# Kernel optimization log

Hardware: AMD Instinct MI355X
Metric: run time of the kernel (lower is better)

The kernel has to match this reference:

```python
import jax, jax.numpy as jnp
import numpy as np

T_STEPS, N, STATE, HID, ACT, C = 32, 64, 64, 128, 32, 96


def setup_inputs() -> dict:
    key = jax.random.key(0)
    ks = jax.random.split(key, 16)
    s = 0.05
    inp = {
        'x': jax.random.normal(ks[0], (T_STEPS, N, STATE), jnp.float32),
        'a': jax.random.normal(ks[1], (T_STEPS, N, ACT), jnp.float32),
        # GRU layer 0 (input state_dim) and layer 1 (input hidden_dim)
        'wih0': jax.random.normal(ks[2], (3 * HID, STATE), jnp.float32) * s,
        'whh0': jax.random.normal(ks[3], (3 * HID, HID), jnp.float32) * s,
        'bih0': jax.random.normal(ks[4], (3 * HID,), jnp.float32) * s,
        'bhh0': jax.random.normal(ks[5], (3 * HID,), jnp.float32) * s,
        'wih1': jax.random.normal(ks[6], (3 * HID, HID), jnp.float32) * s,
        'whh1': jax.random.normal(ks[7], (3 * HID, HID), jnp.float32) * s,
        'bih1': jax.random.normal(ks[8], (3 * HID,), jnp.float32) * s,
        'bhh1': jax.random.normal(ks[9], (3 * HID,), jnp.float32) * s,
        'w1': jax.random.normal(ks[10], (HID, HID + ACT), jnp.float32) * s,
        'b1': jax.random.normal(ks[11], (HID,), jnp.float32) * s,
        'w2': jax.random.normal(ks[12], (1, 2 * HID), jnp.float32) * s,
        'b2': jax.random.normal(ks[13], (1,), jnp.float32) * s,
        'Tm': jax.random.normal(ks[14], (HID, HID, C), jnp.float32),  # init.normal(T,0,1)
    }
    return inp


def _gru_cell(x_t, h, wih, whh, bih, bhh):
    gi = x_t @ wih.T + bih            # (N, 3H)
    gh = h @ whh.T + bhh
    i_r, i_z, i_n = jnp.split(gi, 3, axis=-1)
    h_r, h_z, h_n = jnp.split(gh, 3, axis=-1)
    r = jax.nn.sigmoid(i_r + h_r)
    z = jax.nn.sigmoid(i_z + h_z)
    n = jnp.tanh(i_n + r * h_n)
    return (1.0 - z) * n + z * h


def reference(x, a, wih0, whh0, bih0, bhh0, wih1, whh1, bih1, bhh1, w1, b1, w2, b2, Tm):
    def step(h, x_t):
        h0 = _gru_cell(x_t, h[0], wih0, whh0, bih0, bhh0)
        h1 = _gru_cell(h0, h[1], wih1, whh1, bih1, bhh1)
        return jnp.stack([h0, h1]), h1

    h_init = jnp.zeros((2, N, HID), x.dtype)
    _, p = jax.lax.scan(step, h_init, x)              # (T, N, H)

    fc1 = jax.nn.relu(jnp.concatenate([p, a], -1) @ w1.T + b1)  # (T, N, H)

    Tflat = Tm.reshape(HID, HID * C)

    def batch_discrim(xt):  # xt: (N, H)
        M = (xt @ Tflat).reshape(N, HID, C)           # (N, B, C)
        # pairwise L1 over C: (N, N, B)
        norm = jnp.abs(M[:, None] - M[None, :]).sum(-1)
        o_b = (jnp.exp(-norm).sum(0) - 1.0) / (N - 1)  # (N, B)
        return jnp.concatenate([xt, o_b], 1)          # (N, 2H)

    fc2 = jax.lax.map(batch_discrim, fc1)             # (T, N, 2H)
    prob = jax.nn.sigmoid(fc2 @ w2.T + b2)            # (T, N, 1)
    return prob
```

## Files before the change

kernel.cpp:

```cpp
#include <hip/hip_runtime.h>
#include <hip/hip_fp16.h>
#include <cstdint>

#define T_STEPS 32
#define NB 64
#define STATE 64
#define HID 128
#define ACT 32
#define CDIM 96
#define G3 (3*HID)

typedef __attribute__((ext_vector_type(8))) short short8;
typedef __attribute__((ext_vector_type(4))) float f32x4;
typedef _Float16 h2v __attribute__((ext_vector_type(2)));

__device__ __forceinline__ unsigned short f2bf(float f){
  unsigned int u = __builtin_bit_cast(unsigned int, f);
  u = u + 0x7FFFu + ((u >> 16) & 1u);
  return (unsigned short)(u >> 16);
}
__device__ __forceinline__ unsigned int packh2(float f0, float f1){
  return (unsigned int)__half_as_ushort(__float2half_rn(f0)) |
         ((unsigned int)__half_as_ushort(__float2half_rn(f1)) << 16);
}
__device__ __forceinline__ float sigmoidf_(float x){ return 1.0f/(1.0f + __expf(-x)); }
__device__ __forceinline__ float tanhf_(float x){ float e = __expf(2.0f*x); return (e-1.0f)/(e+1.0f); }

__device__ __forceinline__ float dot2f(float acc, unsigned int a, unsigned int b){
  h2v av = __builtin_bit_cast(h2v, a);
  h2v bv = __builtin_bit_cast(h2v, b);
  return __builtin_amdgcn_fdot2(av, bv, acc, false);
}
__device__ __forceinline__ float l1d(float acc, unsigned int ua, unsigned int ub){
  __half2 a = __builtin_bit_cast(__half2, ua);
  __half2 b = __builtin_bit_cast(__half2, ub);
  __half2 d = __habs2(__hsub2(a, b));
  h2v dv = __builtin_bit_cast(h2v, d);
  h2v ones; ones[0] = (_Float16)1.0f; ones[1] = (_Float16)1.0f;
  return __builtin_amdgcn_fdot2(dv, ones, acc, false);
}
__device__ __forceinline__ float l1d4(float acc, uint4 a, uint4 b){
  acc = l1d(acc, a.x, b.x); acc = l1d(acc, a.y, b.y);
  acc = l1d(acc, a.z, b.z); acc = l1d(acc, a.w, b.w);
  return acc;
}

__global__ void k_prep(const float* __restrict__ Tm, unsigned short* __restrict__ tmh,
                       const float* __restrict__ wih0, const float* __restrict__ whh0,
                       const float* __restrict__ wih1, const float* __restrict__ whh1,
                       const float* __restrict__ w1,
                       unsigned int* __restrict__ wih0p, unsigned int* __restrict__ whh0p,
                       unsigned int* __restrict__ wih1p, unsigned int* __restrict__ whh1p,
                       unsigned int* __restrict__ w1p){
  int tid = threadIdx.x;
  if (blockIdx.x < 128){
    int b = blockIdx.x;
    for (int e = tid; e < HID*CDIM; e += 256){
      int chunk = e / 768;
      int r1 = e - chunk*768;
      int c = r1 >> 3, h = r1 & 7;
      int k = chunk*8 + h;
      tmh[b*(HID*CDIM) + e] = f2bf(Tm[k*(HID*CDIM) + b*CDIM + c]);
    }
  } else {
    int mb = blockIdx.x - 128;
    const float* srcs[5] = {wih0, whh0, wih1, whh1, w1};
    unsigned int* dsts[5] = {wih0p, whh0p, wih1p, whh1p, w1p};
    const int Rs[5]  = {384,384,384,384,128};
    const int K2s[5] = {32,64,64,64,80};
    for (int mm = 0; mm < 5; mm++){
      const float* s = srcs[mm]; unsigned int* d = dsts[mm];
      int R = Rs[mm], K2 = K2s[mm], tot = R*K2;
      for (int e = mb*256 + tid; e < tot; e += 8*256){
        int k2 = e / R, r = e - k2*R;
        d[e] = packh2(s[r*(2*K2) + 2*k2], s[r*(2*K2) + 2*k2 + 1]);
      }
    }
  }
}

__global__ __launch_bounds__(768) void k_gru0(const float* __restrict__ x,
                                              const unsigned int* __restrict__ wih0p,
                                              const unsigned int* __restrict__ whh0p,
                                              const unsigned int* __restrict__ wih1p,
                                              const float* __restrict__ bih0, const float* __restrict__ bhh0,
                                              const float* __restrict__ bih1,
                                              float* __restrict__ gi1g){
  __shared__ __align__(16) unsigned int hl2[64];
  __shared__ __align__(16) unsigned int xall[1024];
  __shared__ float ghl[G3], gil[G3];
  int n = blockIdx.x, tid = threadIdx.x;
  int r = tid >> 1, kh = tid & 1;
  unsigned int wi0[16], wh0[32], wi1[32];
  #pragma unroll
  for (int i = 0; i < 16; i++) wi0[i] = wih0p[(kh*16 + i)*384 + r];
  #pragma unroll
  for (int i = 0; i < 32; i++) wh0[i] = whh0p[(kh*32 + i)*384 + r];
  #pragma unroll
  for (int i = 0; i < 32; i++) wi1[i] = wih1p[(kh*32 + i)*384 + r];
  float bh0 = (kh == 0) ? bhh0[r] : 0.0f;
  float bi0 = (kh == 0) ? bih0[r] : 0.0f;
  float bi1 = (kh == 0) ? bih1[r] : 0.0f;
  for (int e = tid; e < 1024; e += 768){
    int t_ = e >> 5, i = e & 31;
    const float* xp = x + t_*(NB*STATE) + n*STATE + 2*i;
    xall[e] = packh2(xp[0], xp[1]);
  }
  if (tid < 64) hl2[tid] = 0u;
  float hprev = 0.0f;
  __syncthreads();
  const uint4* hl4 = (const uint4*)hl2;
  for (int t = 0; t <= T_STEPS; t++){
    float gh = bh0, gi1 = bi1, gi0 = bi0;
    #pragma unroll
    for (int g = 0; g < 2; g++){
      uint4 hv[4];
      #pragma unroll
      for (int j = 0; j < 4; j++) hv[j] = hl4[kh*8 + g*4 + j];
      #pragma unroll
      for (int j = 0; j < 4; j++){
        gh = dot2f(gh, wh0[g*16 + j*4 + 0], hv[j].x);
        gh = dot2f(gh, wh0[g*16 + j*4 + 1], hv[j].y);
        gh = dot2f(gh, wh0[g*16 + j*4 + 2], hv[j].z);
        gh = dot2f(gh, wh0[g*16 + j*4 + 3], hv[j].w);
        gi1 = dot2f(gi1, wi1[g*16 + j*4 + 0], hv[j].x);
        gi1 = dot2f(gi1, wi1[g*16 + j*4 + 1], hv[j].y);
        gi1 = dot2f(gi1, wi1[g*16 + j*4 + 2], hv[j].z);
        gi1 = dot2f(gi1, wi1[g*16 + j*4 + 3], hv[j].w);
      }
    }
    if (t < T_STEPS){
      const uint4* xl4 = (const uint4*)&xall[t*32];
      #pragma unroll
      for (int j = 0; j < 4; j++){
        uint4 xv = xl4[kh*4 + j];
        gi0 = dot2f(gi0, wi0[j*4 + 0], xv.x);
        gi0 = dot2f(gi0, wi0[j*4 + 1], xv.y);
        gi0 = dot2f(gi0, wi0[j*4 + 2], xv.z);
        gi0 = dot2f(gi0, wi0[j*4 + 3], xv.w);
      }
    }
    gh  += __shfl_xor(gh, 1);
    gi1 += __shfl_xor(gi1, 1);
    gi0 += __shfl_xor(gi0, 1);
    if (kh == 0){
      if (t < T_STEPS){ ghl[r] = gh; gil[r] = gi0; }
      if (t >= 1) gi1g[((t-1)*NB + n)*G3 + r] = gi1;
    }
    __syncthreads();
    if (t < T_STEPS && tid < HID){
      float rg = sigmoidf_(gil[tid]       + ghl[tid]);
      float z  = sigmoidf_(gil[tid+HID]   + ghl[tid+HID]);
      float nn = tanhf_   (gil[tid+2*HID] + rg*ghl[tid+2*HID]);
      float hn = (1.0f - z)*nn + z*hprev;
      hprev = hn;
      ((__half*)hl2)[tid] = __float2half_rn(hn);
    }
    __syncthreads();
  }
}

__global__ __launch_bounds__(768) void k_gru1(const float* __restrict__ a,
                                              const unsigned int* __restrict__ whh1p,
                                              const unsigned int* __restrict__ w1p,
                                              const float* __restrict__ bhh1, const float* __restrict__ b1,
                                              const float* __restrict__ gi1g,
                                              float* __restrict__ fc1f, unsigned short* __restrict__ fc1h){
  __shared__ __align__(16) unsigned int hl2[64];
  __shared__ __align__(16) unsigned int aall[512];
  __shared__ float ghl[G3];
  int n = blockIdx.x, tid = threadIdx.x;
  int r = tid >> 1, kh = tid & 1;
  unsigned int wh1[32];
  #pragma unroll
  for (int i = 0; i < 32; i++) wh1[i] = whh1p[(kh*32 + i)*384 + r];
  unsigned int w1h[32], w1a[8];
  if (r < HID){
    #pragma unroll
    for (int i = 0; i < 32; i++) w1h[i] = w1p[(kh*32 + i)*128 + r];
    #pragma unroll
    for (int i = 0; i < 8; i++)  w1a[i] = w1p[(64 + kh*8 + i)*128 + r];
  }
  float bh1 = (kh == 0) ? bhh1[r] : 0.0f;
  float bf1 = (kh == 0 && r < HID) ? b1[r] : 0.0f;
  for (int e = tid; e < 512; e += 768){
    int t_ = e >> 4, i = e & 15;
    const float* ap = a + t_*(NB*ACT) + n*ACT + 2*i;
    aall[e] = packh2(ap[0], ap[1]);
  }
  if (tid < 64) hl2[tid] = 0u;
  float hprev = 0.0f;
  float g_r = 0.0f, g_z = 0.0f, g_n = 0.0f;
  if (tid < HID){
    const float* gp = gi1g + n*G3 + tid;
    g_r = gp[0]; g_z = gp[HID]; g_n = gp[2*HID];
  }
  __syncthreads();
  const uint4* hl4 = (const uint4*)hl2;
  for (int t = 0; t <= T_STEPS; t++){
    float gh = bh1, fc = bf1;
    bool dofc = (r < HID) && (t >= 1);
    #pragma unroll
    for (int g = 0; g < 2; g++){
      uint4 hv[4];
      #pragma unroll
      for (int j = 0; j < 4; j++) hv[j] = hl4[kh*8 + g*4 + j];
      #pragma unroll
      for (int j = 0; j < 4; j++){
        gh = dot2f(gh, wh1[g*16 + j*4 + 0], hv[j].x);
        gh = dot2f(gh, wh1[g*16 + j*4 + 1], hv[j].y);
        gh = dot2f(gh, wh1[g*16 + j*4 + 2], hv[j].z);
        gh = dot2f(gh, wh1[g*16 + j*4 + 3], hv[j].w);
      }
      if (dofc){
        #pragma unroll
        for (int j = 0; j < 4; j++){
          fc = dot2f(fc, w1h[g*16 + j*4 + 0], hv[j].x);
          fc = dot2f(fc, w1h[g*16 + j*4 + 1], hv[j].y);
          fc = dot2f(fc, w1h[g*16 + j*4 + 2], hv[j].z);
          fc = dot2f(fc, w1h[g*16 + j*4 + 3], hv[j].w);
        }
      }
    }
    if (dofc){
      const uint4* al4 = (const uint4*)&aall[(t-1)*16];
      #pragma unroll
      for (int j = 0; j < 2; j++){
        uint4 av = al4[kh*2 + j];
        fc = dot2f(fc, w1a[j*4 + 0], av.x);
        fc = dot2f(fc, w1a[j*4 + 1], av.y);
        fc = dot2f(fc, w1a[j*4 + 2], av.z);
        fc = dot2f(fc, w1a[j*4 + 3], av.w);
      }
    }
    gh += __shfl_xor(gh, 1);
    fc += __shfl_xor(fc, 1);
    if (kh == 0){
      if (t < T_STEPS) ghl[r] = gh;
      if (t >= 1 && r < HID){
        float v = fmaxf(fc, 0.0f);
        fc1f[((t-1)*NB + n)*HID + r] = v;
        fc1h[(t-1)*8192 + (n>>4)*2048 + (r>>3)*128 + (n&15)*8 + (r&7)] = f2bf(v);
      }
    }
    __syncthreads();
    if (t < T_STEPS && tid < HID){
      float cr = g_r, cz = g_z, cn = g_n;
      int tn2 = (t+1 < T_STEPS) ? t+1 : t;
      const float* gp = gi1g + (tn2*NB + n)*G3 + tid;
      g_r = gp[0]; g_z = gp[HID]; g_n = gp[2*HID];
      float rg = sigmoidf_(cr + ghl[tid]);
      float z  = sigmoidf_(cz + ghl[tid+HID]);
      float nn = tanhf_   (cn + rg*ghl[tid+2*HID]);
      float hn = (1.0f - z)*nn + z*hprev;
      hprev = hn;
      ((__half*)hl2)[tid] = __float2half_rn(hn);
    }
    __syncthreads();
  }
}

__global__ __launch_bounds__(256) void k_disc(const unsigned short* __restrict__ fc1h,
                                              const unsigned short* __restrict__ tmh,
                                              float* __restrict__ O){
  __shared__ __align__(16) __half Mh[64*104];
  __shared__ float ps[64*18];
  int b = blockIdx.x, t = blockIdx.y;
  int tid = threadIdx.x;
  int wave = tid >> 6, lane = tid & 63, m = lane & 15, quad = lane >> 4;
  const uint4* Ag = (const uint4*)(fc1h + t*8192);
  const uint4* Bg = (const uint4*)(tmh + b*(CDIM*HID));
  uint4 a4[4];
  #pragma unroll
  for (int kk = 0; kk < 4; kk++) a4[kk] = Ag[wave*256 + (kk*4 + quad)*16 + m];
  f32x4 acc[6];
  #pragma unroll
  for (int i = 0; i < 6; i++) acc[i] = (f32x4)(0.0f);
  #pragma unroll
  for (int kk = 0; kk < 4; kk++){
    short8 av = __builtin_bit_cast(short8, a4[kk]);
    #pragma unroll
    for (int nt = 0; nt < 6; nt++){
      uint4 b4 = Bg[(kk*4 + quad)*96 + nt*16 + m];
      acc[nt] = __builtin_amdgcn_mfma_f32_16x16x32_bf16(av, __builtin_bit_cast(short8, b4), acc[nt], 0, 0, 0);
    }
  }
  #pragma unroll
  for (int nt = 0; nt < 6; nt++){
    #pragma unroll
    for (int rr = 0; rr < 4; rr++){
      Mh[(rr*16 + wave*4 + quad)*104 + nt*16 + m] = __float2half(acc[nt][rr]);
    }
  }
  __syncthreads();
  const uint4* M4 = (const uint4*)Mh;
  if (tid < 240){
    int chalf = tid & 1, tp = tid >> 1;
    int rnd = tp >> 3, slot = tp & 7;
    int ta, tb;
    if (slot == 0){ ta = 15; tb = rnd; }
    else {
      ta = rnd + slot;      if (ta >= 15) ta -= 15;
      tb = rnd + 15 - slot; if (tb >= 15) tb -= 15;
    }
    float facc[16];
    #pragma unroll
    for (int p = 0; p < 16; p++) facc[p] = 0.0f;
    auto doChunk = [&](int c){
      int ch = chalf*6 + c;
      uint4 av[4], bv[4];
      #pragma unroll
      for (int s = 0; s < 4; s++){
        av[s] = M4[(s*16 + ta)*13 + ch];
        bv[s] = M4[(s*16 + tb)*13 + ch];
      }
      #pragma unroll
      for (int i = 0; i < 4; i++)
        #pragma unroll
        for (int j = 0; j < 4; j++)
          facc[i*4+j] = l1d4(facc[i*4+j], av[i], bv[j]);
    };
    doChunk(0); doChunk(1);
    bool big1 = true;
    #pragma unroll
    for (int p = 0; p < 16; p++) big1 = big1 && (facc[p] > 14.0f);
    if (!big1){
      doChunk(2); doChunk(3);
      bool big2 = true;
      #pragma unroll
      for (int p = 0; p < 16; p++) big2 = big2 && (facc[p] > 14.0f);
      if (!big2){ doChunk(4); doChunk(5); }
    }
    float tot[16];
    #pragma unroll
    for (int p = 0; p < 16; p++) tot[p] = facc[p] + __shfl_xor(facc[p], 1);
    if (chalf == 0){
      #pragma unroll
      for (int i = 0; i < 4; i++){
        float s = 0.0f;
        #pragma unroll
        for (int j = 0; j < 4; j++) s += __expf(-tot[i*4+j]);
        ps[(ta*4 + i)*18 + tb] = s;
      }
    } else {
      #pragma unroll
      for (int j = 0; j < 4; j++){
        float s = 0.0f;
        #pragma unroll
        for (int i = 0; i < 4; i++) s += __expf(-tot[i*4+j]);
        ps[(tb*4 + j)*18 + ta] = s;
      }
    }
  } else {
    int ta = tid - 240;
    float f6[6];
    #pragma unroll
    for (int p = 0; p < 6; p++) f6[p] = 0.0f;
    auto doChunkS = [&](int ch){
      uint4 rv[4];
      #pragma unroll
      for (int s = 0; s < 4; s++) rv[s] = M4[(s*16 + ta)*13 + ch];
      f6[0] = l1d4(f6[0], rv[0], rv[1]);
      f6[1] = l1d4(f6[1], rv[0], rv[2]);
      f6[2] = l1d4(f6[2], rv[0], rv[3]);
      f6[3] = l1d4(f6[3], rv[1], rv[2]);
      f6[4] = l1d4(f6[4], rv[1], rv[3]);
      f6[5] = l1d4(f6[5], rv[2], rv[3]);
    };
    doChunkS(0); doChunkS(1); doChunkS(2);
    bool big1 = true;
    #pragma unroll
    for (int p = 0; p < 6; p++) big1 = big1 && (f6[p] > 14.0f);
    if (!big1){
      doChunkS(3); doChunkS(4); doChunkS(5);
      bool big2 = true;
      #pragma unroll
      for (int p = 0; p < 6; p++) big2 = big2 && (f6[p] > 14.0f);
      if (!big2){
        doChunkS(6); doChunkS(7); doChunkS(8);
        doChunkS(9); doChunkS(10); doChunkS(11);
      }
    }
    float e01 = __expf(-f6[0]), e02 = __expf(-f6[1]), e03 = __expf(-f6[2]);
    float e12 = __expf(-f6[3]), e13 = __expf(-f6[4]), e23 = __expf(-f6[5]);
    ps[(ta*4 + 0)*18 + ta] = e01 + e02 + e03;
    ps[(ta*4 + 1)*18 + ta] = e01 + e12 + e13;
    ps[(ta*4 + 2)*18 + ta] = e02 + e12 + e23;
    ps[(ta*4 + 3)*18 + ta] = e03 + e13 + e23;
  }
  __syncthreads();
  if (tid < NB){
    float s = 0.0f;
    #pragma unroll
    for (int k = 0; k < 16; k++) s += ps[tid*18 + k];
    O[(t*HID + b)*NB + tid] = s*(1.0f/63.0f);
  }
}

__global__ __launch_bounds__(256) void k_final(const float* __restrict__ fc1f, const float* __restrict__ O,
                                               const float* __restrict__ w2, const float* __restrict__ b2,
                                               float* __restrict__ out){
  __shared__ float ol[NB*HID];
  __shared__ float fl[NB*130];
  __shared__ float wl[2*HID + 2];
  int t = blockIdx.x, tid = threadIdx.x;
  for (int i = tid; i < NB*HID; i += 256) ol[i] = O[t*NB*HID + i];
  for (int i = tid; i < NB*HID; i += 256){ int n = i >> 7, h = i & 127; fl[n*130 + h] = fc1f[t*NB*HID + i]; }
  if (tid < 2*HID) wl[tid] = w2[tid];
  if (tid == 0) wl[2*HID] = b2[0];
  __syncthreads();
  if (tid < NB){
    float acc = wl[2*HID];
    #pragma unroll 8
    for (int h = 0; h < HID; h++) acc += fl[tid*130 + h]*wl[h];
    #pragma unroll 8
    for (int b = 0; b < HID; b++) acc += ol[b*NB + tid]*wl[HID + b];
    out[t*NB + tid] = sigmoidf_(acc);
  }
}

extern "C" void kernel_launch(void* const* d_in, const int* in_sizes, int n_in,
                              void* d_out, int out_size, void* d_ws, size_t ws_size,
                              hipStream_t stream){
  const float* x    = (const float*)d_in[0];
  const float* a    = (const float*)d_in[1];
  const float* wih0 = (const float*)d_in[2];
  const float* whh0 = (const float*)d_in[3];
  const float* bih0 = (const float*)d_in[4];
  const float* bhh0 = (const float*)d_in[5];
  const float* wih1 = (const float*)d_in[6];
  const float* whh1 = (const float*)d_in[7];
  const float* bih1 = (const float*)d_in[8];
  const float* bhh1 = (const float*)d_in[9];
  const float* w1   = (const float*)d_in[10];
  const float* b1   = (const float*)d_in[11];
  const float* w2   = (const float*)d_in[12];
  const float* b2   = (const float*)d_in[13];
  const float* Tm   = (const float*)d_in[14];
  float* ws = (float*)d_ws;
  float* gi1g = ws;
  float* fc1f = ws + 786432;
  float* Ows  = ws + 1048576;
  unsigned short* fc1h = (unsigned short*)(ws + 1310720);
  unsigned short* tmh  = (unsigned short*)(ws + 1441792);
  unsigned int* wih0p = (unsigned int*)(ws + 2228224);
  unsigned int* whh0p = (unsigned int*)(ws + 2240512);
  unsigned int* wih1p = (unsigned int*)(ws + 2265088);
  unsigned int* whh1p = (unsigned int*)(ws + 2289664);
  unsigned int* w1p   = (unsigned int*)(ws + 2314240);
  float* out = (float*)d_out;

  k_prep<<<dim3(136), dim3(256), 0, stream>>>(Tm, tmh, wih0, whh0, wih1, whh1, w1,
                                              wih0p, whh0p, wih1p, whh1p, w1p);
  k_gru0<<<dim3(NB), dim3(768), 0, stream>>>(x, wih0p, whh0p, wih1p, bih0, bhh0, bih1, gi1g);
  k_gru1<<<dim3(NB), dim3(768), 0, stream>>>(a, whh1p, w1p, bhh1, b1, gi1g, fc1f, fc1h);
  k_disc<<<dim3(HID, T_STEPS), dim3(256), 0, stream>>>(fc1h, tmh, Ows);
  k_final<<<dim3(T_STEPS), dim3(256), 0, stream>>>(fc1f, Ows, w2, b2, out);
}
```

Measured before the change: 212.8 us.

## Fuse both GRU layers into one kernel and move fc1 to an MFMA kernel

Merges the two GRU recurrence kernels into a single per-sample kernel that runs both layers each timestep. This removes the gi1 global round trip and one launch, but adds an extra barrier phase per step and more register pressure from holding four weight sets. The fc1 layer now runs as a separate bf16 MFMA kernel over all timesteps, with the action inputs prepacked in k_prep. k_disc processes 4 timesteps per block, which reuses the Tm tile but gives fewer blocks, and k_final reads the bf16 fc1 output instead of a float copy.

```diff
diff --git a/kernel.cpp b/kernel.cpp
--- a/kernel.cpp
+++ b/kernel.cpp
@@ -19,6 +19,9 @@
   u = u + 0x7FFFu + ((u >> 16) & 1u);
   return (unsigned short)(u >> 16);
 }
+__device__ __forceinline__ float bf2f(unsigned short u){
+  unsigned int v = ((unsigned int)u) << 16; return __builtin_bit_cast(float, v);
+}
 __device__ __forceinline__ unsigned int packh2(float f0, float f1){
   return (unsigned int)__half_as_ushort(__float2half_rn(f0)) |
          ((unsigned int)__half_as_ushort(__float2half_rn(f1)) << 16);
@@ -48,13 +51,14 @@
 __global__ void k_prep(const float* __restrict__ Tm, unsigned short* __restrict__ tmh,
                        const float* __restrict__ wih0, const float* __restrict__ whh0,
                        const float* __restrict__ wih1, const float* __restrict__ whh1,
-                       const float* __restrict__ w1,
+                       const float* __restrict__ w1, const float* __restrict__ a,
                        unsigned int* __restrict__ wih0p, unsigned int* __restrict__ whh0p,
                        unsigned int* __restrict__ wih1p, unsigned int* __restrict__ whh1p,
-                       unsigned int* __restrict__ w1p){
+                       unsigned short* __restrict__ w1f, unsigned short* __restrict__ h1af){
   int tid = threadIdx.x;
-  if (blockIdx.x < 128){
-    int b = blockIdx.x;
+  int bx = blockIdx.x;
+  if (bx < 128){
+    int b = bx;
     for (int e = tid; e < HID*CDIM; e += 256){
       int chunk = e / 768;
       int r1 = e - chunk*768;
@@ -62,201 +66,178 @@
       int k = chunk*8 + h;
       tmh[b*(HID*CDIM) + e] = f2bf(Tm[k*(HID*CDIM) + b*CDIM + c]);
     }
+  } else if (bx < 136){
+    int mb = bx - 128;
+    const float* srcs[4] = {wih0, whh0, wih1, whh1};
+    unsigned int* dsts[4] = {wih0p, whh0p, wih1p, whh1p};
+    const int K2s[4] = {32,64,64,64};
+    for (int mm = 0; mm < 4; mm++){
+      const float* s = srcs[mm]; unsigned int* d = dsts[mm];
+      int K2 = K2s[mm], tot = 384*K2;
+      for (int e = mb*256 + tid; e < tot; e += 8*256){
+        int k2 = e / 384, r = e - k2*384;
+        d[e] = packh2(s[r*(2*K2) + 2*k2], s[r*(2*K2) + 2*k2 + 1]);
+      }
+    }
+  } else if (bx < 140){
+    int mb = bx - 136;
+    for (int e = mb*256 + tid; e < 20480; e += 4*256){
+      int kchunk = e >> 10, rem = e & 1023;
+      int col = rem >> 3, j = rem & 7;
+      w1f[e] = f2bf(w1[col*160 + kchunk*8 + j]);
+    }
   } else {
-    int mb = blockIdx.x - 128;
-    const float* srcs[5] = {wih0, whh0, wih1, whh1, w1};
-    unsigned int* dsts[5] = {wih0p, whh0p, wih1p, whh1p, w1p};
-    const int Rs[5]  = {384,384,384,384,128};
-    const int K2s[5] = {32,64,64,64,80};
-    for (int mm = 0; mm < 5; mm++){
-      const float* s = srcs[mm]; unsigned int* d = dsts[mm];
-      int R = Rs[mm], K2 = K2s[mm], tot = R*K2;
-      for (int e = mb*256 + tid; e < tot; e += 8*256){
-        int k2 = e / R, r = e - k2*R;
-        d[e] = packh2(s[r*(2*K2) + 2*k2], s[r*(2*K2) + 2*k2 + 1]);
-      }
-    }
-  }
-}
-
-__global__ __launch_bounds__(768) void k_gru0(const float* __restrict__ x,
-                                              const unsigned int* __restrict__ wih0p,
-                                              const unsigned int* __restrict__ whh0p,
-                                              const unsigned int* __restrict__ wih1p,
-                                              const float* __restrict__ bih0, const float* __restrict__ bhh0,
-                                              const float* __restrict__ bih1,
-                                              float* __restrict__ gi1g){
-  __shared__ __align__(16) unsigned int hl2[64];
+    int mb = bx - 140;
+    for (int e = mb*256 + tid; e < 65536; e += 12*256){
+      int t = e >> 11, rem = e & 2047;
+      int n = rem >> 5, c = rem & 31;
+      int pos = t*10240 + (n>>4)*2560 + (16 + (c>>3))*128 + (n&15)*8 + (c&7);
+      h1af[pos] = f2bf(a[t*(NB*ACT) + n*ACT + c]);
+    }
+  }
+}
+
+__global__ __launch_bounds__(768, 3) void k_gruF(const float* __restrict__ x,
+                                                 const unsigned int* __restrict__ wih0p,
+                                                 const unsigned int* __restrict__ whh0p,
+                                                 const unsigned int* __restrict__ wih1p,
+                                                 const unsigned int* __restrict__ whh1p,
+                                                 const float* __restrict__ bih0, const float* __restrict__ bhh0,
+                                                 const float* __restrict__ bih1, const float* __restrict__ bhh1,
+                                                 unsigned short* __restrict__ h1af){
+  __shared__ __align__(16) unsigned int h0l[64];
+  __shared__ __align__(16) unsigned int h1l[64];
   __shared__ __align__(16) unsigned int xall[1024];
-  __shared__ float ghl[G3], gil[G3];
+  __shared__ float A0[G3], B0[G3], C1[G3];
   int n = blockIdx.x, tid = threadIdx.x;
   int r = tid >> 1, kh = tid & 1;
-  unsigned int wi0[16], wh0[32], wi1[32];
+  unsigned int wi0[16], wh0[32], wi1[32], wh1[32];
   #pragma unroll
   for (int i = 0; i < 16; i++) wi0[i] = wih0p[(kh*16 + i)*384 + r];
   #pragma unroll
   for (int i = 0; i < 32; i++) wh0[i] = whh0p[(kh*32 + i)*384 + r];
   #pragma unroll
   for (int i = 0; i < 32; i++) wi1[i] = wih1p[(kh*32 + i)*384 + r];
-  float bh0 = (kh == 0) ? bhh0[r] : 0.0f;
-  float bi0 = (kh == 0) ? bih0[r] : 0.0f;
-  float bi1 = (kh == 0) ? bih1[r] : 0.0f;
+  #pragma unroll
+  for (int i = 0; i < 32; i++) wh1[i] = whh1p[(kh*32 + i)*384 + r];
+  float bh0v = (kh == 0) ? bhh0[r] : 0.0f;
+  float bi0v = (kh == 0) ? bih0[r] : 0.0f;
+  float bi1v = (kh == 0) ? bih1[r] : 0.0f;
+  float bh1v = (kh == 0) ? bhh1[r] : 0.0f;
   for (int e = tid; e < 1024; e += 768){
     int t_ = e >> 5, i = e & 31;
     const float* xp = x + t_*(NB*STATE) + n*STATE + 2*i;
     xall[e] = packh2(xp[0], xp[1]);
   }
-  if (tid < 64) hl2[tid] = 0u;
-  float hprev = 0.0f;
+  if (tid < 64){ h0l[tid] = 0u; h1l[tid] = 0u; }
+  float h0prev = 0.0f, h1prev = 0.0f;
   __syncthreads();
-  const uint4* hl4 = (const uint4*)hl2;
-  for (int t = 0; t <= T_STEPS; t++){
-    float gh = bh0, gi1 = bi1, gi0 = bi0;
+  const uint4* h04 = (const uint4*)h0l;
+  const uint4* h14 = (const uint4*)h1l;
+  const uint4* xl4 = (const uint4*)xall;
+  for (int t = 0; t < T_STEPS; t++){
+    float gh0 = bh0v, gi0 = bi0v, gh1 = bh1v;
+    #pragma unroll
+    for (int g = 0; g < 2; g++){
+      uint4 hv0[4], hv1[4];
+      #pragma unroll
+      for (int j = 0; j < 4; j++){ hv0[j] = h04[kh*8 + g*4 + j]; hv1[j] = h14[kh*8 + g*4 + j]; }
+      #pragma unroll
+      for (int j = 0; j < 4; j++){
+        gh0 = dot2f(gh0, wh0[g*16 + j*4 + 0], hv0[j].x);
+        gh0 = dot2f(gh0, wh0[g*16 + j*4 + 1], hv0[j].y);
+        gh0 = dot2f(gh0, wh0[g*16 + j*4 + 2], hv0[j].z);
+        gh0 = dot2f(gh0, wh0[g*16 + j*4 + 3], hv0[j].w);
+        gh1 = dot2f(gh1, wh1[g*16 + j*4 + 0], hv1[j].x);
+        gh1 = dot2f(gh1, wh1[g*16 + j*4 + 1], hv1[j].y);
+        gh1 = dot2f(gh1, wh1[g*16 + j*4 + 2], hv1[j].z);
+        gh1 = dot2f(gh1, wh1[g*16 + j*4 + 3], hv1[j].w);
+      }
+    }
+    #pragma unroll
+    for (int j = 0; j < 4; j++){
+      uint4 xv = xl4[t*8 + kh*4 + j];
+      gi0 = dot2f(gi0, wi0[j*4 + 0], xv.x);
+      gi0 = dot2f(gi0, wi0[j*4 + 1], xv.y);
+      gi0 = dot2f(gi0, wi0[j*4 + 2], xv.z);
+      gi0 = dot2f(gi0, wi0[j*4 + 3], xv.w);
+    }
+    gh0 += __shfl_xor(gh0, 1);
+    gi0 += __shfl_xor(gi0, 1);
+    gh1 += __shfl_xor(gh1, 1);
+    if (kh == 0){ A0[r] = gh0; B0[r] = gi0; C1[r] = gh1; }
+    __syncthreads();
+    if (tid < HID){
+      float rg = sigmoidf_(B0[tid]       + A0[tid]);
+      float z  = sigmoidf_(B0[tid+HID]   + A0[tid+HID]);
+      float nn = tanhf_   (B0[tid+2*HID] + rg*A0[tid+2*HID]);
+      float hn = (1.0f - z)*nn + z*h0prev;
+      h0prev = hn;
+      ((__half*)h0l)[tid] = __float2half_rn(hn);
+    }
+    __syncthreads();
+    float gi1 = bi1v;
     #pragma unroll
     for (int g = 0; g < 2; g++){
       uint4 hv[4];
       #pragma unroll
-      for (int j = 0; j < 4; j++) hv[j] = hl4[kh*8 + g*4 + j];
+      for (int j = 0; j < 4; j++) hv[j] = h04[kh*8 + g*4 + j];
       #pragma unroll
       for (int j = 0; j < 4; j++){
-        gh = dot2f(gh, wh0[g*16 + j*4 + 0], hv[j].x);
-        gh = dot2f(gh, wh0[g*16 + j*4 + 1], hv[j].y);
-        gh = dot2f(gh, wh0[g*16 + j*4 + 2], hv[j].z);
-        gh = dot2f(gh, wh0[g*16 + j*4 + 3], hv[j].w);
         gi1 = dot2f(gi1, wi1[g*16 + j*4 + 0], hv[j].x);
         gi1 = dot2f(gi1, wi1[g*16 + j*4 + 1], hv[j].y);
         gi1 = dot2f(gi1, wi1[g*16 + j*4 + 2], hv[j].z);
         gi1 = dot2f(gi1, wi1[g*16 + j*4 + 3], hv[j].w);
       }
     }
-    if (t < T_STEPS){
-      const uint4* xl4 = (const uint4*)&xall[t*32];
-      #pragma unroll
-      for (int j = 0; j < 4; j++){
-        uint4 xv = xl4[kh*4 + j];
-        gi0 = dot2f(gi0, wi0[j*4 + 0], xv.x);
-        gi0 = dot2f(gi0, wi0[j*4 + 1], xv.y);
-        gi0 = dot2f(gi0, wi0[j*4 + 2], xv.z);
-        gi0 = dot2f(gi0, wi0[j*4 + 3], xv.w);
-      }
-    }
-    gh  += __shfl_xor(gh, 1);
     gi1 += __shfl_xor(gi1, 1);
-    gi0 += __shfl_xor(gi0, 1);
-    if (kh == 0){
-      if (t < T_STEPS){ ghl[r] = gh; gil[r] = gi0; }
-      if (t >= 1) gi1g[((t-1)*NB + n)*G3 + r] = gi1;
-    }
-    __syncthreads();
-    if (t < T_STEPS && tid < HID){
-      float rg = sigmoidf_(gil[tid]       + ghl[tid]);
-      float z  = sigmoidf_(gil[tid+HID]   + ghl[tid+HID]);
-      float nn = tanhf_   (gil[tid+2*HID] + rg*ghl[tid+2*HID]);
-      float hn = (1.0f - z)*nn + z*hprev;
-      hprev = hn;
-      ((__half*)hl2)[tid] = __float2half_rn(hn);
-    }
-    __syncthreads();
-  }
-}
-
-__global__ __launch_bounds__(768) void k_gru1(const float* __restrict__ a,
-                                              const unsigned int* __restrict__ whh1p,
-                                              const unsigned int* __restrict__ w1p,
-                                              const float* __restrict__ bhh1, const float* __restrict__ b1,
-                                              const float* __restrict__ gi1g,
-                                              float* __restrict__ fc1f, unsigned short* __restrict__ fc1h){
-  __shared__ __align__(16) unsigned int hl2[64];
-  __shared__ __align__(16) unsigned int aall[512];
-  __shared__ float ghl[G3];
-  int n = blockIdx.x, tid = threadIdx.x;
-  int r = tid >> 1, kh = tid & 1;
-  unsigned int wh1[32];
-  #pragma unroll
-  for (int i = 0; i < 32; i++) wh1[i] = whh1p[(kh*32 + i)*384 + r];
-  unsigned int w1h[32], w1a[8];
-  if (r < HID){
-    #pragma unroll
-    for (int i = 0; i < 32; i++) w1h[i] = w1p[(kh*32 + i)*128 + r];
-    #pragma unroll
-    for (int i = 0; i < 8; i++)  w1a[i] = w1p[(64 + kh*8 + i)*128 + r];
-  }
-  float bh1 = (kh == 0) ? bhh1[r] : 0.0f;
-  float bf1 = (kh == 0 && r < HID) ? b1[r] : 0.0f;
-  for (int e = tid; e < 512; e += 768){
-    int t_ = e >> 4, i = e & 15;
-    const float* ap = a + t_*(NB*ACT) + n*ACT + 2*i;
-    aall[e] = packh2(ap[0], ap[1]);
-  }
-  if (tid < 64) hl2[tid] = 0u;
-  float hprev = 0.0f;
-  float g_r = 0.0f, g_z = 0.0f, g_n = 0.0f;
-  if (tid < HID){
-    const float* gp = gi1g + n*G3 + tid;
-    g_r = gp[0]; g_z = gp[HID]; g_n = gp[2*HID];
+    if (kh == 0) B0[r] = gi1;
+    __syncthreads();
+    if (tid < HID){
+      float rg = sigmoidf_(B0[tid]       + C1[tid]);
+      float z  = sigmoidf_(B0[tid+HID]   + C1[tid+HID]);
+      float nn = tanhf_   (B0[tid+2*HID] + rg*C1[tid+2*HID]);
+      float hn = (1.0f - z)*nn + z*h1prev;
+      h1prev = hn;
+      ((__half*)h1l)[tid] = __float2half_rn(hn);
+      h1af[t*10240 + (n>>4)*2560 + (tid>>3)*128 + (n&15)*8 + (tid&7)] = f2bf(hn);
+    }
+    __syncthreads();
+  }
+}
+
+__global__ __launch_bounds__(256) void k_fc1(const unsigned short* __restrict__ h1af,
+                                             const unsigned short* __restrict__ w1f,
+                                             const float* __restrict__ b1,
+                                             unsigned short* __restrict__ fc1h){
+  __shared__ float b1s[128];
+  int t = blockIdx.x, tid = threadIdx.x;
+  int wave = tid >> 6, lane = tid & 63, m = lane & 15, quad = lane >> 4;
+  if (tid < 128) b1s[tid] = b1[tid];
+  const uint4* A4 = (const uint4*)(h1af + t*10240);
+  const uint4* B4 = (const uint4*)w1f;
+  f32x4 acc[8];
+  #pragma unroll
+  for (int i = 0; i < 8; i++) acc[i] = (f32x4)(0.0f);
+  #pragma unroll
+  for (int ks = 0; ks < 5; ks++){
+    uint4 av = A4[wave*320 + (ks*4 + quad)*16 + m];
+    short8 avs = __builtin_bit_cast(short8, av);
+    #pragma unroll
+    for (int nt = 0; nt < 8; nt++){
+      uint4 bv = B4[(ks*4 + quad)*128 + nt*16 + m];
+      acc[nt] = __builtin_amdgcn_mfma_f32_16x16x32_bf16(avs, __builtin_bit_cast(short8, bv), acc[nt], 0, 0, 0);
+    }
   }
   __syncthreads();
-  const uint4* hl4 = (const uint4*)hl2;
-  for (int t = 0; t <= T_STEPS; t++){
-    float gh = bh1, fc = bf1;
-    bool dofc = (r < HID) && (t >= 1);
-    #pragma unroll
-    for (int g = 0; g < 2; g++){
-      uint4 hv[4];
-      #pragma unroll
-      for (int j = 0; j < 4; j++) hv[j] = hl4[kh*8 + g*4 + j];
-      #pragma unroll
-      for (int j = 0; j < 4; j++){
-        gh = dot2f(gh, wh1[g*16 + j*4 + 0], hv[j].x);
-        gh = dot2f(gh, wh1[g*16 + j*4 + 1], hv[j].y);
-        gh = dot2f(gh, wh1[g*16 + j*4 + 2], hv[j].z);
-        gh = dot2f(gh, wh1[g*16 + j*4 + 3], hv[j].w);
-      }
-      if (dofc){
-        #pragma unroll
-        for (int j = 0; j < 4; j++){
-          fc = dot2f(fc, w1h[g*16 + j*4 + 0], hv[j].x);
-          fc = dot2f(fc, w1h[g*16 + j*4 + 1], hv[j].y);
-          fc = dot2f(fc, w1h[g*16 + j*4 + 2], hv[j].z);
-          fc = dot2f(fc, w1h[g*16 + j*4 + 3], hv[j].w);
-        }
-      }
-    }
-    if (dofc){
-      const uint4* al4 = (const uint4*)&aall[(t-1)*16];
-      #pragma unroll
-      for (int j = 0; j < 2; j++){
-        uint4 av = al4[kh*2 + j];
-        fc = dot2f(fc, w1a[j*4 + 0], av.x);
-        fc = dot2f(fc, w1a[j*4 + 1], av.y);
-        fc = dot2f(fc, w1a[j*4 + 2], av.z);
-        fc = dot2f(fc, w1a[j*4 + 3], av.w);
-      }
-    }
-    gh += __shfl_xor(gh, 1);
-    fc += __shfl_xor(fc, 1);
-    if (kh == 0){
-      if (t < T_STEPS) ghl[r] = gh;
-      if (t >= 1 && r < HID){
-        float v = fmaxf(fc, 0.0f);
-        fc1f[((t-1)*NB + n)*HID + r] = v;
-        fc1h[(t-1)*8192 + (n>>4)*2048 + (r>>3)*128 + (n&15)*8 + (r&7)] = f2bf(v);
-      }
-    }
-    __syncthreads();
-    if (t < T_STEPS && tid < HID){
-      float cr = g_r, cz = g_z, cn = g_n;
-      int tn2 = (t+1 < T_STEPS) ? t+1 : t;
-      const float* gp = gi1g + (tn2*NB + n)*G3 + tid;
-      g_r = gp[0]; g_z = gp[HID]; g_n = gp[2*HID];
-      float rg = sigmoidf_(cr + ghl[tid]);
-      float z  = sigmoidf_(cz + ghl[tid+HID]);
-      float nn = tanhf_   (cn + rg*ghl[tid+2*HID]);
-      float hn = (1.0f - z)*nn + z*hprev;
-      hprev = hn;
-      ((__half*)hl2)[tid] = __float2half_rn(hn);
-    }
-    __syncthreads();
+  #pragma unroll
+  for (int nt = 0; nt < 8; nt++){
+    float bj = b1s[nt*16 + m];
+    #pragma unroll
+    for (int rr = 0; rr < 4; rr++){
+      float v = fmaxf(acc[nt][rr] + bj, 0.0f);
+      fc1h[t*8192 + wave*2048 + (nt*2 + (m>>3))*128 + (quad*4 + rr)*8 + (m&7)] = f2bf(v);
+    }
   }
 }
 
@@ -265,154 +246,162 @@
                                               float* __restrict__ O){
   __shared__ __align__(16) __half Mh[64*104];
   __shared__ float ps[64*18];
-  int b = blockIdx.x, t = blockIdx.y;
+  int b = blockIdx.x;
   int tid = threadIdx.x;
   int wave = tid >> 6, lane = tid & 63, m = lane & 15, quad = lane >> 4;
-  const uint4* Ag = (const uint4*)(fc1h + t*8192);
   const uint4* Bg = (const uint4*)(tmh + b*(CDIM*HID));
-  uint4 a4[4];
-  #pragma unroll
-  for (int kk = 0; kk < 4; kk++) a4[kk] = Ag[wave*256 + (kk*4 + quad)*16 + m];
-  f32x4 acc[6];
-  #pragma unroll
-  for (int i = 0; i < 6; i++) acc[i] = (f32x4)(0.0f);
-  #pragma unroll
-  for (int kk = 0; kk < 4; kk++){
-    short8 av = __builtin_bit_cast(short8, a4[kk]);
+  #pragma unroll 1
+  for (int tt = 0; tt < 4; tt++){
+    int t = blockIdx.y*4 + tt;
+    const uint4* Ag = (const uint4*)(fc1h + t*8192);
+    uint4 a4[4];
+    #pragma unroll
+    for (int kk = 0; kk < 4; kk++) a4[kk] = Ag[wave*256 + (kk*4 + quad)*16 + m];
+    f32x4 acc[6];
+    #pragma unroll
+    for (int i = 0; i < 6; i++) acc[i] = (f32x4)(0.0f);
+    #pragma unroll
+    for (int kk = 0; kk < 4; kk++){
+      short8 av = __builtin_bit_cast(short8, a4[kk]);
+      #pragma unroll
+      for (int nt = 0; nt < 6; nt++){
+        uint4 b4 = Bg[(kk*4 + quad)*96 + nt*16 + m];
+        acc[nt] = __builtin_amdgcn_mfma_f32_16x16x32_bf16(av, __builtin_bit_cast(short8, b4), acc[nt], 0, 0, 0);
+      }
+    }
+    __syncthreads();
     #pragma unroll
     for (int nt = 0; nt < 6; nt++){
-      uint4 b4 = Bg[(kk*4 + quad)*96 + nt*16 + m];
-      acc[nt] = __builtin_amdgcn_mfma_f32_16x16x32_bf16(av, __builtin_bit_cast(short8, b4), acc[nt], 0, 0, 0);
-    }
-  }
-  #pragma unroll
-  for (int nt = 0; nt < 6; nt++){
-    #pragma unroll
-    for (int rr = 0; rr < 4; rr++){
-      Mh[(rr*16 + wave*4 + quad)*104 + nt*16 + m] = __float2half(acc[nt][rr]);
-    }
-  }
-  __syncthreads();
-  const uint4* M4 = (const uint4*)Mh;
-  if (tid < 240){
-    int chalf = tid & 1, tp = tid >> 1;
-    int rnd = tp >> 3, slot = tp & 7;
-    int ta, tb;
-    if (slot == 0){ ta = 15; tb = rnd; }
-    else {
-      ta = rnd + slot;      if (ta >= 15) ta -= 15;
-      tb = rnd + 15 - slot; if (tb >= 15) tb -= 15;
-    }
-    float facc[16];
-    #pragma unroll
-    for (int p = 0; p < 16; p++) facc[p] = 0.0f;
-    auto doChunk = [&](int c){
-      int ch = chalf*6 + c;
-      uint4 av[4], bv[4];
-      #pragma unroll
-      for (int s = 0; s < 4; s++){
-        av[s] = M4[(s*16 + ta)*13 + ch];
-        bv[s] = M4[(s*16 + tb)*13 + ch];
-      }
-      #pragma unroll
-      for (int i = 0; i < 4; i++)
-        #pragma unroll
-        for (int j = 0; j < 4; j++)
-          facc[i*4+j] = l1d4(facc[i*4+j], av[i], bv[j]);
-    };
-    doChunk(0); doChunk(1);
-    bool big1 = true;
-    #pragma unroll
-    for (int p = 0; p < 16; p++) big1 = big1 && (facc[p] > 14.0f);
-    if (!big1){
-      doChunk(2); doChunk(3);
-      bool big2 = true;
-      #pragma unroll
-      for (int p = 0; p < 16; p++) big2 = big2 && (facc[p] > 14.0f);
-      if (!big2){ doChunk(4); doChunk(5); }
-    }
-    float tot[16];
-    #pragma unroll
-    for (int p = 0; p < 16; p++) tot[p] = facc[p] + __shfl_xor(facc[p], 1);
-    if (chalf == 0){
-      #pragma unroll
-      for (int i = 0; i < 4; i++){
-        float s = 0.0f;
-        #pragma unroll
-        for (int j = 0; j < 4; j++) s += __expf(-tot[i*4+j]);
-        ps[(ta*4 + i)*18 + tb] = s;
+      #pragma unroll
+      for (int rr = 0; rr < 4; rr++){
+        Mh[(rr*16 + wave*4 + quad)*104 + nt*16 + m] = __float2half(acc[nt][rr]);
+      }
+    }
+    __syncthreads();
+    const uint4* M4 = (const uint4*)Mh;
+    if (tid < 240){
+      int chalf = tid & 1, tp = tid >> 1;
+      int rnd = tp >> 3, slot = tp & 7;
+      int ta, tb;
+      if (slot == 0){ ta = 15; tb = rnd; }
+      else {
+        ta = rnd + slot;      if (ta >= 15) ta -= 15;
+        tb = rnd + 15 - slot; if (tb >= 15) tb -= 15;
+      }
+      float facc[16];
+      #pragma unroll
+      for (int p = 0; p < 16; p++) facc[p] = 0.0f;
+      auto doChunk = [&](int c){
+        int ch = chalf*6 + c;
+        uint4 av[4], bv[4];
+        #pragma unroll
+        for (int s = 0; s < 4; s++){
+          av[s] = M4[(s*16 + ta)*13 + ch];
+          bv[s] = M4[(s*16 + tb)*13 + ch];
+        }
+        #pragma unroll
+        for (int i = 0; i < 4; i++)
+          #pragma unroll
+          for (int j = 0; j < 4; j++)
+            facc[i*4+j] = l1d4(facc[i*4+j], av[i], bv[j]);
+      };
+      doChunk(0); doChunk(1);
+      bool big1 = true;
+      #pragma unroll
+      for (int p = 0; p < 16; p++) big1 = big1 && (facc[p] > 14.0f);
+      if (!big1){
+        doChunk(2); doChunk(3);
+        bool big2 = true;
+        #pragma unroll
+        for (int p = 0; p < 16; p++) big2 = big2 && (facc[p] > 14.0f);
+        if (!big2){ doChunk(4); doChunk(5); }
+      }
+      float tot[16];
+      #pragma unroll
+      for (int p = 0; p < 16; p++) tot[p] = facc[p] + __shfl_xor(facc[p], 1);
+      if (chalf == 0){
+        #pragma unroll
+        for (int i = 0; i < 4; i++){
+          float s = 0.0f;
+          #pragma unroll
+          for (int j = 0; j < 4; j++) s += __expf(-tot[i*4+j]);
+          ps[(ta*4 + i)*18 + tb] = s;
+        }
+      } else {
+        #pragma unroll
+        for (int j = 0; j < 4; j++){
+          float s = 0.0f;
+          #pragma unroll
+          for (int i = 0; i < 4; i++) s += __expf(-tot[i*4+j]);
+          ps[(tb*4 + j)*18 + ta] = s;
+        }
       }
     } else {
-      #pragma unroll
-      for (int j = 0; j < 4; j++){
-        float s = 0.0f;
-        #pragma unroll
-        for (int i = 0; i < 4; i++) s += __expf(-tot[i*4+j]);
-        ps[(tb*4 + j)*18 + ta] = s;
-      }
-    }
-  } else {
-    int ta = tid - 240;
-    float f6[6];
-    #pragma unroll
-    for (int p = 0; p < 6; p++) f6[p] = 0.0f;
-    auto doChunkS = [&](int ch){
-      uint4 rv[4];
-      #pragma unroll
-      for (int s = 0; s < 4; s++) rv[s] = M4[(s*16 + ta)*13 + ch];
-      f6[0] = l1d4(f6[0], rv[0], rv[1]);
-      f6[1] = l1d4(f6[1], rv[0], rv[2]);
-      f6[2] = l1d4(f6[2], rv[0], rv[3]);
-      f6[3] = l1d4(f6[3], rv[1], rv[2]);
-      f6[4] = l1d4(f6[4], rv[1], rv[3]);
-      f6[5] = l1d4(f6[5], rv[2], rv[3]);
-    };
-    doChunkS(0); doChunkS(1); doChunkS(2);
-    bool big1 = true;
-    #pragma unroll
-    for (int p = 0; p < 6; p++) big1 = big1 && (f6[p] > 14.0f);
-    if (!big1){
-      doChunkS(3); doChunkS(4); doChunkS(5);
-      bool big2 = true;
-      #pragma unroll
-      for (int p = 0; p < 6; p++) big2 = big2 && (f6[p] > 14.0f);
-      if (!big2){
-        doChunkS(6); doChunkS(7); doChunkS(8);
-        doChunkS(9); doChunkS(10); doChunkS(11);
-      }
-    }
-    float e01 = __expf(-f6[0]), e02 = __expf(-f6[1]), e03 = __expf(-f6[2]);
-    float e12 = __expf(-f6[3]), e13 = __expf(-f6[4]), e23 = __expf(-f6[5]);
-    ps[(ta*4 + 0)*18 + ta] = e01 + e02 + e03;
-    ps[(ta*4 + 1)*18 + ta] = e01 + e12 + e13;
-    ps[(ta*4 + 2)*18 + ta] = e02 + e12 + e23;
-    ps[(ta*4 + 3)*18 + ta] = e03 + e13 + e23;
-  }
-  __syncthreads();
-  if (tid < NB){
-    float s = 0.0f;
-    #pragma unroll
-    for (int k = 0; k < 16; k++) s += ps[tid*18 + k];
-    O[(t*HID + b)*NB + tid] = s*(1.0f/63.0f);
-  }
-}
-
-__global__ __launch_bounds__(256) void k_final(const float* __restrict__ fc1f, const float* __restrict__ O,
+      int ta = tid - 240;
+      float f6[6];
+      #pragma unroll
+      for (int p = 0; p < 6; p++) f6[p] = 0.0f;
+      auto doChunkS = [&](int ch){
+        uint4 rv[4];
+        #pragma unroll
+        for (int s = 0; s < 4; s++) rv[s] = M4[(s*16 + ta)*13 + ch];
+        f6[0] = l1d4(f6[0], rv[0], rv[1]);
+        f6[1] = l1d4(f6[1], rv[0], rv[2]);
+        f6[2] = l1d4(f6[2], rv[0], rv[3]);
+        f6[3] = l1d4(f6[3], rv[1], rv[2]);
+        f6[4] = l1d4(f6[4], rv[1], rv[3]);
+        f6[5] = l1d4(f6[5], rv[2], rv[3]);
+      };
+      doChunkS(0); doChunkS(1); doChunkS(2);
+      bool big1 = true;
+      #pragma unroll
+      for (int p = 0; p < 6; p++) big1 = big1 && (f6[p] > 14.0f);
+      if (!big1){
+        doChunkS(3); doChunkS(4); doChunkS(5);
+        bool big2 = true;
+        #pragma unroll
+        for (int p = 0; p < 6; p++) big2 = big2 && (f6[p] > 14.0f);
+        if (!big2){
+          doChunkS(6); doChunkS(7); doChunkS(8);
+          doChunkS(9); doChunkS(10); doChunkS(11);
+        }
+      }
+      float e01 = __expf(-f6[0]), e02 = __expf(-f6[1]), e03 = __expf(-f6[2]);
+      float e12 = __expf(-f6[3]), e13 = __expf(-f6[4]), e23 = __expf(-f6[5]);
+      ps[(ta*4 + 0)*18 + ta] = e01 + e02 + e03;
+      ps[(ta*4 + 1)*18 + ta] = e01 + e12 + e13;
+      ps[(ta*4 + 2)*18 + ta] = e02 + e12 + e23;
+      ps[(ta*4 + 3)*18 + ta] = e03 + e13 + e23;
+    }
+    __syncthreads();
+    if (tid < NB){
+      float s = 0.0f;
+      #pragma unroll
+      for (int k = 0; k < 16; k++) s += ps[tid*18 + k];
+      O[(t*HID + b)*NB + tid] = s*(1.0f/63.0f);
+    }
+  }
+}
+
+__global__ __launch_bounds__(256) void k_final(const unsigned short* __restrict__ fc1h,
+                                               const float* __restrict__ O,
                                                const float* __restrict__ w2, const float* __restrict__ b2,
                                                float* __restrict__ out){
   __shared__ float ol[NB*HID];
-  __shared__ float fl[NB*130];
+  __shared__ unsigned short fr[8192];
   __shared__ float wl[2*HID + 2];
   int t = blockIdx.x, tid = threadIdx.x;
   for (int i = tid; i < NB*HID; i += 256) ol[i] = O[t*NB*HID + i];
-  for (int i = tid; i < NB*HID; i += 256){ int n = i >> 7, h = i & 127; fl[n*130 + h] = fc1f[t*NB*HID + i]; }
+  const uint4* Fg = (const uint4*)(fc1h + t*8192);
+  for (int i = tid; i < 1024; i += 256) ((uint4*)fr)[i] = Fg[i];
   if (tid < 2*HID) wl[tid] = w2[tid];
   if (tid == 0) wl[2*HID] = b2[0];
   __syncthreads();
   if (tid < NB){
     float acc = wl[2*HID];
+    int base = (tid>>4)*2048 + (tid&15)*8;
     #pragma unroll 8
-    for (int h = 0; h < HID; h++) acc += fl[tid*130 + h]*wl[h];
+    for (int j = 0; j < HID; j++) acc += bf2f(fr[base + (j>>3)*128 + (j&7)])*wl[j];
     #pragma unroll 8
     for (int b = 0; b < HID; b++) acc += ol[b*NB + tid]*wl[HID + b];
     out[t*NB + tid] = sigmoidf_(acc);
@@ -438,22 +427,22 @@
   const float* b2   = (const float*)d_in[13];
   const float* Tm   = (const float*)d_in[14];
   float* ws = (float*)d_ws;
-  float* gi1g = ws;
-  float* fc1f = ws + 786432;
-  float* Ows  = ws + 1048576;
-  unsigned short* fc1h = (unsigned short*)(ws + 1310720);
-  unsigned short* tmh  = (unsigned short*)(ws + 1441792);
-  unsigned int* wih0p = (unsigned int*)(ws + 2228224);
-  unsigned int* whh0p = (unsigned int*)(ws + 2240512);
-  unsigned int* wih1p = (unsigned int*)(ws + 2265088);
-  unsigned int* whh1p = (unsigned int*)(ws + 2289664);
-  unsigned int* w1p   = (unsigned int*)(ws + 2314240);
+  float* Ows = ws;
+  unsigned int* wih0p = (unsigned int*)(ws + 262144);
+  unsigned int* whh0p = (unsigned int*)(ws + 274432);
+  unsigned int* wih1p = (unsigned int*)(ws + 299008);
+  unsigned int* whh1p = (unsigned int*)(ws + 323584);
+  unsigned short* tmh  = (unsigned short*)(ws + 348160);
+  unsigned short* fc1h = (unsigned short*)(ws + 1134592);
+  unsigned short* h1af = (unsigned short*)(ws + 1265664);
+  unsigned short* w1f  = (unsigned short*)(ws + 1429504);
   float* out = (float*)d_out;
 
-  k_prep<<<dim3(136), dim3(256), 0, stream>>>(Tm, tmh, wih0, whh0, wih1, whh1, w1,
-                                              wih0p, whh0p, wih1p, whh1p, w1p);
-  k_gru0<<<dim3(NB), dim3(768), 0, stream>>>(x, wih0p, whh0p, wih1p, bih0, bhh0, bih1, gi1g);
-  k_gru1<<<dim3(NB), dim3(768), 0, stream>>>(a, whh1p, w1p, bhh1, b1, gi1g, fc1f, fc1h);
-  k_disc<<<dim3(HID, T_STEPS), dim3(256), 0, stream>>>(fc1h, tmh, Ows);
-  k_final<<<dim3(T_STEPS), dim3(256), 0, stream>>>(fc1f, Ows, w2, b2, out);
-}
+  k_prep<<<dim3(152), dim3(256), 0, stream>>>(Tm, tmh, wih0, whh0, wih1, whh1, w1, a,
+                                              wih0p, whh0p, wih1p, whh1p, w1f, h1af);
+  k_gruF<<<dim3(NB), dim3(768), 0, stream>>>(x, wih0p, whh0p, wih1p, whh1p,
+                                             bih0, bhh0, bih1, bhh1, h1af);
+  k_fc1<<<dim3(T_STEPS), dim3(256), 0, stream>>>(h1af, w1f, b1, fc1h);
+  k_disc<<<dim3(HID, T_STEPS/4), dim3(256), 0, stream>>>(fc1h, tmh, Ows);
+  k_final<<<dim3(T_STEPS), dim3(256), 0, stream>>>(fc1h, Ows, w2, b2, out);
+}
```

Result: slower. 245.0 us (+15.1%).
